# Optimization experiments

Measured on AMD Instinct MI355X. Metric: run time of the kernel, lower is better.

The kernel has to match this reference:

```python
import jax, jax.numpy as jnp
import numpy as np

N = 2_000_000
WIDTH, HEIGHT = 1920, 1080
ZNEAR, ZFAR = 0.01, 100.0
TAN_FOVX = 0.5773503  # 60 deg horizontal FoV
TAN_FOVY = TAN_FOVX * HEIGHT / WIDTH


def _camera():
    # Row-vector convention: x_view = x_h @ world2view (translation in last row).
    w2v = np.eye(4, dtype=np.float32)
    w2v[3, 2] = 5.0  # push scene 5 units in front of the camera
    P = np.zeros((4, 4), dtype=np.float32)
    P[0, 0] = 1.0 / TAN_FOVX
    P[1, 1] = 1.0 / TAN_FOVY
    P[2, 2] = ZFAR / (ZFAR - ZNEAR)
    P[3, 2] = -(ZFAR * ZNEAR) / (ZFAR - ZNEAR)
    P[2, 3] = 1.0
    full = w2v @ P
    return jnp.asarray(w2v), jnp.asarray(full)


def setup_inputs() -> dict:
    key = jax.random.key(0)
    ks = jax.random.split(key, 5)
    w2v, full = _camera()
    return dict(
        points=jax.random.normal(ks[0], (N, 3), jnp.float32) * 2.0,
        colors=jax.random.uniform(ks[1], (N, 3), jnp.float32),
        opacity=jax.random.normal(ks[2], (N,), jnp.float32),
        scales=jax.random.uniform(ks[3], (N, 3), jnp.float32, minval=0.01, maxval=0.2),
        quaternions=jax.random.normal(ks[4], (N, 4), jnp.float32),
        world2view=w2v,
        full_proj_transform=full,
        tan_fovX=jnp.full((1,), TAN_FOVX, jnp.float32),
        tan_fovY=jnp.full((1,), TAN_FOVY, jnp.float32),
        focal_x=jnp.full((1,), WIDTH / (2.0 * TAN_FOVX), jnp.float32),
        focal_y=jnp.full((1,), HEIGHT / (2.0 * TAN_FOVY), jnp.float32),
        width=WIDTH,
        height=HEIGHT,
    )


def _quat_to_rot(q):
    q = q / jnp.linalg.norm(q, axis=-1, keepdims=True)
    w, x, y, z = q[:, 0], q[:, 1], q[:, 2], q[:, 3]
    R = jnp.stack([
        1 - 2 * (y * y + z * z), 2 * (x * y - w * z), 2 * (x * z + w * y),
        2 * (x * y + w * z), 1 - 2 * (x * x + z * z), 2 * (y * z - w * x),
        2 * (x * z - w * y), 2 * (y * z + w * x), 1 - 2 * (x * x + y * y),
    ], axis=-1)
    return R.reshape(-1, 3, 3)


def reference(points, colors, opacity, scales, quaternions, world2view,
              full_proj_transform, tan_fovX, tan_fovY, focal_x, focal_y,
              width, height):
    n = points.shape[0]
    # --- 3D covariance: Sigma = (R S)(R S)^T ---
    R = _quat_to_rot(quaternions)                      # [N,3,3]
    M = R * scales[:, None, :]                         # R @ diag(s)
    cov3d = jnp.einsum('nij,nkj->nik', M, M)           # [N,3,3]

    # --- view / clip transforms (row-vector convention) ---
    ph = jnp.concatenate([points, jnp.ones((n, 1), points.dtype)], axis=1)
    pview = ph @ world2view                            # [N,4]
    zview = pview[:, 2]
    in_view = zview >= 0.2                             # frustum (near-plane) cull

    pclip = ph @ full_proj_transform
    pndc = pclip[:, :3] / pclip[:, 3:4]
    px = ((pndc[:, 0] + 1.0) * width - 1.0) * 0.5      # ndc2Pix
    py = ((pndc[:, 1] + 1.0) * height - 1.0) * 0.5

    # --- 2D covariance via projection Jacobian (EWA splatting) ---
    xc = jnp.clip(pview[:, 0] / zview, -1.3 * tan_fovX, 1.3 * tan_fovX) * zview
    yc = jnp.clip(pview[:, 1] / zview, -1.3 * tan_fovY, 1.3 * tan_fovY) * zview
    z2 = zview * zview
    zero = jnp.zeros_like(zview)
    J = jnp.stack([
        focal_x / zview, zero, -(focal_x * xc) / z2,
        zero, focal_y / zview, -(focal_y * yc) / z2,
        zero, zero, zero,
    ], axis=-1).reshape(-1, 3, 3)                      # [N,3,3]
    W = world2view[:3, :3].T
    T = jnp.einsum('nij,jk->nik', J, W)
    cov2d = jnp.einsum('nij,njk,nlk->nil', T, cov3d, T)[:, :2, :2]

    # --- analytic 2x2 inverse ---
    c00, c01 = cov2d[:, 0, 0], cov2d[:, 0, 1]
    c10, c11 = cov2d[:, 1, 0], cov2d[:, 1, 1]
    det = c00 * c11 - c01 * c10
    det_safe = jnp.where(jnp.abs(det) < 1e-6, 1e-6, det)
    inv_cov = jnp.stack([c11, -c01, -c10, c00], axis=-1) / det_safe[:, None]

    # --- extent / radius: 3 sigma of dominant eigenvalue ---
    mid = 0.5 * (c00 + c11)
    inter = jnp.maximum(mid * mid - det, 0.1)
    lam = mid + jnp.sqrt(inter)
    radius = jnp.ceil(3.0 * jnp.sqrt(jnp.maximum(lam, 0.0)))

    min_x = jnp.floor(px - radius)
    min_y = jnp.floor(py - radius)
    max_x = jnp.ceil(px + radius)
    max_y = jnp.ceil(py + radius)

    # --- depth sort; culled gaussians keyed to +inf (fixed-shape stand-in for boolean gather) ---
    depth_key = jnp.where(in_view, zview, jnp.float32(jnp.inf))
    order = jnp.argsort(depth_key)

    packed = jnp.concatenate([
        px[:, None], py[:, None], zview[:, None],
        cov2d.reshape(n, 4), inv_cov,
        radius[:, None],
        min_x[:, None], min_y[:, None], max_x[:, None], max_y[:, None],
        colors, jax.nn.sigmoid(opacity)[:, None],
        in_view.astype(points.dtype)[:, None],
    ], axis=1)                                          # [N,21]
    return packed[order]
```

## Files before the change

### kernel.cpp

```cpp
#include <hip/hip_runtime.h>
#include <hip/hip_bf16.h>
#include <math.h>

#define BLK   256
#define IPT   16
#define TILE  (BLK * IPT)
#define BINS  256
#define PASSES 4
#define SCT   4096

__global__ __launch_bounds__(256) void k_keys(const float* __restrict__ pts,
                                              const float* __restrict__ w2v,
                                              int N,
                                              unsigned* __restrict__ keys,
                                              unsigned* __restrict__ idx)
{
    int i = blockIdx.x * 256 + threadIdx.x;
    if (i >= N) return;
    float x = pts[3*i+0], y = pts[3*i+1], z = pts[3*i+2];
    float zv = x*w2v[2] + y*w2v[6] + z*w2v[10] + w2v[14];
    float key = (zv >= 0.2f) ? zv : __int_as_float(0x7f800000);
    unsigned u = __float_as_uint(key);
    u ^= (u & 0x80000000u) ? 0xFFFFFFFFu : 0x80000000u;
    keys[i] = u;
    idx[i]  = (unsigned)i;
}

__global__ __launch_bounds__(256) void k_hist8(const unsigned* __restrict__ keys,
                                               int N, int numTiles, int shift,
                                               unsigned* __restrict__ hist)
{
    __shared__ unsigned bins[BINS];
    int t = threadIdx.x, b = blockIdx.x;
    bins[t] = 0;
    __syncthreads();
    int base = b * TILE;
    for (int k = 0; k < IPT; ++k) {
        int l = base + k * BLK + t;
        if (l < N) atomicAdd(&bins[(keys[l] >> shift) & 255u], 1u);
    }
    __syncthreads();
    hist[t * numTiles + b] = bins[t];
}

__global__ __launch_bounds__(256) void k_scanA(const unsigned* __restrict__ h, int E,
                                               unsigned* __restrict__ bsum)
{
    __shared__ unsigned red[256];
    int t = threadIdx.x;
    int base = blockIdx.x * SCT + t * 16;
    unsigned acc = 0;
    if (base + 16 <= E) {
        const uint4* p = (const uint4*)(h + base);
        #pragma unroll
        for (int q = 0; q < 4; ++q) { uint4 v = p[q]; acc += v.x + v.y + v.z + v.w; }
    } else {
        for (int k = 0; k < 16; ++k) { int i = base + k; if (i < E) acc += h[i]; }
    }
    red[t] = acc;
    __syncthreads();
    for (int off = 128; off > 0; off >>= 1) {
        if (t < off) red[t] += red[t + off];
        __syncthreads();
    }
    if (t == 0) bsum[blockIdx.x] = red[0];
}

__global__ __launch_bounds__(256) void k_scanB(unsigned* __restrict__ h, int E,
                                               const unsigned* __restrict__ bsum)
{
    __shared__ unsigned tsum[256];
    __shared__ unsigned boff_s;
    int t = threadIdx.x, b = blockIdx.x;
    int base = b * SCT + t * 16;

    if (t == 0) { unsigned o = 0; for (int i = 0; i < b; ++i) o += bsum[i]; boff_s = o; }

    unsigned v[16];
    bool full = (base + 16 <= E);
    if (full) {
        const uint4* p = (const uint4*)(h + base);
        #pragma unroll
        for (int q = 0; q < 4; ++q) { uint4 u = p[q]; v[4*q]=u.x; v[4*q+1]=u.y; v[4*q+2]=u.z; v[4*q+3]=u.w; }
    } else {
        for (int k = 0; k < 16; ++k) { int i = base + k; v[k] = (i < E) ? h[i] : 0u; }
    }
    unsigned acc = 0;
    #pragma unroll
    for (int k = 0; k < 16; ++k) { unsigned x = v[k]; v[k] = acc; acc += x; }
    tsum[t] = acc;
    __syncthreads();
    for (int off = 1; off < 256; off <<= 1) {
        unsigned u = (t >= off) ? tsum[t - off] : 0u;
        __syncthreads();
        tsum[t] += u;
        __syncthreads();
    }
    unsigned add = boff_s + ((t == 0) ? 0u : tsum[t - 1]);
    if (full) {
        uint4* p = (uint4*)(h + base);
        #pragma unroll
        for (int q = 0; q < 4; ++q)
            p[q] = make_uint4(v[4*q] + add, v[4*q+1] + add, v[4*q+2] + add, v[4*q+3] + add);
    } else {
        for (int k = 0; k < 16; ++k) { int i = base + k; if (i < E) h[i] = v[k] + add; }
    }
}

__global__ __launch_bounds__(256) void k_scatter8(const unsigned* __restrict__ keys,
                                                  const unsigned* __restrict__ vals,
                                                  int N, int numTiles, int shift,
                                                  const unsigned* __restrict__ hist,
                                                  unsigned* __restrict__ okeys,
                                                  unsigned* __restrict__ ovals)
{
    __shared__ unsigned short cnt[64 * BINS];
    __shared__ unsigned tileBase[BINS];
    __shared__ unsigned digStartL[BINS];
    __shared__ unsigned tscan[BINS];
    __shared__ unsigned stage_k[TILE];
    __shared__ unsigned stage_v[TILE];

    int t = threadIdx.x, b = blockIdx.x;
    int w = t >> 6, l = t & 63;
    int base = b * TILE;
    int nvalid = N - base; if (nvalid < 0) nvalid = 0; if (nvalid > TILE) nvalid = TILE;

    unsigned* c32 = (unsigned*)cnt;
    #pragma unroll
    for (int i = 0; i < (64 * BINS / 2) / BLK; ++i) c32[i * BLK + t] = 0;
    __syncthreads();

    unsigned k_[IPT], v_[IPT];
    unsigned char r_[IPT], d_[IPT];

    #pragma unroll
    for (int it = 0; it < IPT; ++it) {
        int e = base + it * BLK + t;
        bool ok = e < N;
        k_[it] = ok ? keys[e] : 0u;
        v_[it] = ok ? vals[e] : 0u;
    }

    #pragma unroll
    for (int it = 0; it < IPT; ++it) {
        int e = base + it * BLK + t;
        bool ok = e < N;
        unsigned d = (k_[it] >> shift) & 255u;
        unsigned long long mm = __ballot(ok);
        #pragma unroll
        for (int bb = 0; bb < 8; ++bb) {
            unsigned long long bal = __ballot(ok && ((d >> bb) & 1u));
            mm &= ((d >> bb) & 1u) ? bal : ~bal;
        }
        unsigned long long below = mm & ((1ull << l) - 1ull);
        unsigned rk = (unsigned)__popcll(below);
        if (ok && rk == 0)
            cnt[(it * 4 + w) * BINS + d] = (unsigned short)__popcll(mm);
        r_[it] = (unsigned char)rk;
        d_[it] = (unsigned char)d;
    }
    __syncthreads();

    {
        unsigned run = 0;
        #pragma unroll
        for (int s = 0; s < 64; ++s) {
            unsigned h = cnt[s * BINS + t];
            cnt[s * BINS + t] = (unsigned short)run;
            run += h;
        }
        tscan[t] = run;
        tileBase[t] = hist[t * numTiles + b];
    }
    __syncthreads();

    for (int off = 1; off < 256; off <<= 1) {
        unsigned u = (t >= off) ? tscan[t - off] : 0u;
        __syncthreads();
        tscan[t] += u;
        __syncthreads();
    }
    digStartL[t] = (t == 0) ? 0u : tscan[t - 1];
    __syncthreads();

    #pragma unroll
    for (int it = 0; it < IPT; ++it) {
        int e = base + it * BLK + t;
        if (e >= N) continue;
        unsigned d = d_[it];
        unsigned lp = digStartL[d] + (unsigned)cnt[(it * 4 + w) * BINS + d] + (unsigned)r_[it];
        stage_k[lp] = k_[it];
        stage_v[lp] = v_[it];
    }
    __syncthreads();

    #pragma unroll
    for (int it = 0; it < IPT; ++it) {
        int p = it * BLK + t;
        if (p >= nvalid) continue;
        unsigned kk = stage_k[p];
        unsigned d = (kk >> shift) & 255u;
        unsigned pos = tileBase[d] + ((unsigned)p - digStartL[d]);
        okeys[pos] = kk;
        ovals[pos] = stage_v[p];
    }
}

__device__ __forceinline__ void compute_row(int j,
                                            const float* __restrict__ pts,
                                            const float* __restrict__ cols,
                                            const float* __restrict__ opa,
                                            const float* __restrict__ scl,
                                            const float* __restrict__ qt,
                                            const float* __restrict__ w2v,
                                            const float* __restrict__ fpm,
                                            float tanX, float tanY, float fx, float fy,
                                            float Wf, float Hf,
                                            float* r )
{
    float x = pts[3*j+0], y = pts[3*j+1], z = pts[3*j+2];

    float qw = qt[4*j+0], qx = qt[4*j+1], qy = qt[4*j+2], qz = qt[4*j+3];
    float qn = sqrtf(qw*qw + qx*qx + qy*qy + qz*qz);
    qw /= qn; qx /= qn; qy /= qn; qz /= qn;
    float R00 = 1.f - 2.f*(qy*qy + qz*qz), R01 = 2.f*(qx*qy - qw*qz), R02 = 2.f*(qx*qz + qw*qy);
    float R10 = 2.f*(qx*qy + qw*qz), R11 = 1.f - 2.f*(qx*qx + qz*qz), R12 = 2.f*(qy*qz - qw*qx);
    float R20 = 2.f*(qx*qz - qw*qy), R21 = 2.f*(qy*qz + qw*qx), R22 = 1.f - 2.f*(qx*qx + qy*qy);

    float s0 = scl[3*j+0], s1 = scl[3*j+1], s2 = scl[3*j+2];
    float M00=R00*s0, M01=R01*s1, M02=R02*s2;
    float M10=R10*s0, M11=R11*s1, M12=R12*s2;
    float M20=R20*s0, M21=R21*s1, M22=R22*s2;
    float C00=M00*M00+M01*M01+M02*M02;
    float C01=M00*M10+M01*M11+M02*M12;
    float C02=M00*M20+M01*M21+M02*M22;
    float C11=M10*M10+M11*M11+M12*M12;
    float C12=M10*M20+M11*M21+M12*M22;
    float C22=M20*M20+M21*M21+M22*M22;

    float pvx = x*w2v[0] + y*w2v[4] + z*w2v[8]  + w2v[12];
    float pvy = x*w2v[1] + y*w2v[5] + z*w2v[9]  + w2v[13];
    float zv  = x*w2v[2] + y*w2v[6] + z*w2v[10] + w2v[14];
    bool in_view = (zv >= 0.2f);

    float cx = x*fpm[0] + y*fpm[4] + z*fpm[8]  + fpm[12];
    float cy = x*fpm[1] + y*fpm[5] + z*fpm[9]  + fpm[13];
    float cw = x*fpm[3] + y*fpm[7] + z*fpm[11] + fpm[15];
    float ndx = cx / cw, ndy = cy / cw;
    float px = ((ndx + 1.f) * Wf - 1.f) * 0.5f;
    float py = ((ndy + 1.f) * Hf - 1.f) * 0.5f;

    float lx = 1.3f * tanX, ly = 1.3f * tanY;
    float xc = fminf(fmaxf(pvx / zv, -lx), lx) * zv;
    float yc = fminf(fmaxf(pvy / zv, -ly), ly) * zv;
    float z2 = zv * zv;
    float J00 = fx / zv, J02 = -(fx * xc) / z2;
    float J11 = fy / zv, J12 = -(fy * yc) / z2;

    float T00 = J00*w2v[0] + J02*w2v[2];
    float T01 = J00*w2v[4] + J02*w2v[6];
    float T02 = J00*w2v[8] + J02*w2v[10];
    float T10 = J11*w2v[1] + J12*w2v[2];
    float T11 = J11*w2v[5] + J12*w2v[6];
    float T12 = J11*w2v[9] + J12*w2v[10];

    float V00 = T00*C00 + T01*C01 + T02*C02;
    float V01 = T00*C01 + T01*C11 + T02*C12;
    float V02 = T00*C02 + T01*C12 + T02*C22;
    float V10 = T10*C00 + T11*C01 + T12*C02;
    float V11 = T10*C01 + T11*C11 + T12*C12;
    float V12 = T10*C02 + T11*C12 + T12*C22;
    float c00 = V00*T00 + V01*T01 + V02*T02;
    float c01 = V00*T10 + V01*T11 + V02*T12;
    float c10 = V10*T00 + V11*T01 + V12*T02;
    float c11 = V10*T10 + V11*T11 + V12*T12;

    float det = c00*c11 - c01*c10;
    float det_safe = (fabsf(det) < 1e-6f) ? 1e-6f : det;
    float i00 =  c11 / det_safe, i01 = -c01 / det_safe;
    float i10 = -c10 / det_safe, i11 =  c00 / det_safe;
    float mid = 0.5f * (c00 + c11);
    float inter = fmaxf(mid*mid - det, 0.1f);
    float lam = mid + sqrtf(inter);
    float radius = ceilf(3.0f * sqrtf(fmaxf(lam, 0.0f)));
    float min_x = floorf(px - radius), min_y = floorf(py - radius);
    float max_x = ceilf(px + radius),  max_y = ceilf(py + radius);
    float op = 1.0f / (1.0f + expf(-opa[j]));

    r[0]=px; r[1]=py; r[2]=zv;
    r[3]=c00; r[4]=c01; r[5]=c10; r[6]=c11;
    r[7]=i00; r[8]=i01; r[9]=i10; r[10]=i11;
    r[11]=radius; r[12]=min_x; r[13]=min_y; r[14]=max_x; r[15]=max_y;
    r[16]=cols[3*j+0]; r[17]=cols[3*j+1]; r[18]=cols[3*j+2];
    r[19]=op; r[20]= in_view ? 1.0f : 0.0f;
}

__global__ __launch_bounds__(256) void k_rows(const float* __restrict__ pts,
                                              const float* __restrict__ cols,
                                              const float* __restrict__ opa,
                                              const float* __restrict__ scl,
                                              const float* __restrict__ qt,
                                              const float* __restrict__ w2v,
                                              const float* __restrict__ fpm,
                                              const float* __restrict__ tanx_p,
                                              const float* __restrict__ tany_p,
                                              const float* __restrict__ fx_p,
                                              const float* __restrict__ fy_p,
                                              const int* __restrict__ wp,
                                              const int* __restrict__ hp,
                                              float* __restrict__ rows, int N)
{
    int i = blockIdx.x * 256 + threadIdx.x;
    if (i >= N) return;
    float r[21];
    compute_row(i, pts, cols, opa, scl, qt, w2v, fpm,
                tanx_p[0], tany_p[0], fx_p[0], fy_p[0],
                (float)wp[0], (float)hp[0], r);
    float4* rp = (float4*)(rows + (size_t)i * 24);
    rp[0] = make_float4(r[0],  r[1],  r[2],  r[3]);
    rp[1] = make_float4(r[4],  r[5],  r[6],  r[7]);
    rp[2] = make_float4(r[8],  r[9],  r[10], r[11]);
    rp[3] = make_float4(r[12], r[13], r[14], r[15]);
    rp[4] = make_float4(r[16], r[17], r[18], r[19]);
    rp[5] = make_float4(r[20], 0.f,   0.f,   0.f);
}

__global__ __launch_bounds__(256) void k_perm(const unsigned* __restrict__ order,
                                              const float* __restrict__ rows,
                                              float* __restrict__ out, int N)
{
    __shared__ float srow[256 * 21];
    int i = blockIdx.x * 256 + threadIdx.x;
    if (i < N) {
        int j = (int)order[i];
        const float4* rp = (const float4*)(rows + (size_t)j * 24);
        float4 a = rp[0], b4 = rp[1], c4 = rp[2], d4 = rp[3], e4 = rp[4];
        float  f = rows[(size_t)j * 24 + 20];
        float* r = &srow[threadIdx.x * 21];
        r[0]=a.x;  r[1]=a.y;  r[2]=a.z;  r[3]=a.w;
        r[4]=b4.x; r[5]=b4.y; r[6]=b4.z; r[7]=b4.w;
        r[8]=c4.x; r[9]=c4.y; r[10]=c4.z; r[11]=c4.w;
        r[12]=d4.x; r[13]=d4.y; r[14]=d4.z; r[15]=d4.w;
        r[16]=e4.x; r[17]=e4.y; r[18]=e4.z; r[19]=e4.w;
        r[20]=f;
    }
    __syncthreads();
    int blockBase = blockIdx.x * 256;
    int valid = N - blockBase; if (valid > 256) valid = 256;
    if (valid > 0) {
        float* dst = out + (size_t)blockBase * 21;
        for (int u = threadIdx.x; u < valid * 21; u += 256) dst[u] = srow[u];
    }
}

__global__ __launch_bounds__(256) void k_emit(const unsigned* __restrict__ order,
                                              const float* __restrict__ pts,
                                              const float* __restrict__ cols,
                                              const float* __restrict__ opa,
                                              const float* __restrict__ scl,
                                              const float* __restrict__ qt,
                                              const float* __restrict__ w2v,
                                              const float* __restrict__ fpm,
                                              const float* __restrict__ tanx_p,
                                              const float* __restrict__ tany_p,
                                              const float* __restrict__ fx_p,
                                              const float* __restrict__ fy_p,
                                              const int* __restrict__ wp,
                                              const int* __restrict__ hp,
                                              float* __restrict__ out, int N)
{
    __shared__ float srow[256 * 21];
    int i = blockIdx.x * 256 + threadIdx.x;
    if (i < N) {
        int j = (int)order[i];
        compute_row(j, pts, cols, opa, scl, qt, w2v, fpm,
                    tanx_p[0], tany_p[0], fx_p[0], fy_p[0],
                    (float)wp[0], (float)hp[0], &srow[threadIdx.x * 21]);
    }
    __syncthreads();
    int blockBase = blockIdx.x * 256;
    int valid = N - blockBase; if (valid > 256) valid = 256;
    if (valid > 0) {
        float* dst = out + (size_t)blockBase * 21;
        for (int u = threadIdx.x; u < valid * 21; u += 256) dst[u] = srow[u];
    }
}

extern "C" void kernel_launch(void* const* d_in, const int* in_sizes, int n_in,
                              void* d_out, int out_size, void* d_ws, size_t ws_size,
                              hipStream_t stream)
{
    const float* pts  = (const float*)d_in[0];
    const float* cols = (const float*)d_in[1];
    const float* opa  = (const float*)d_in[2];
    const float* scl  = (const float*)d_in[3];
    const float* qt   = (const float*)d_in[4];
    const float* w2v  = (const float*)d_in[5];
    const float* fpm  = (const float*)d_in[6];
    const float* tanx = (const float*)d_in[7];
    const float* tany = (const float*)d_in[8];
    const float* fx   = (const float*)d_in[9];
    const float* fy   = (const float*)d_in[10];
    const int*   wp   = (const int*)d_in[11];
    const int*   hp   = (const int*)d_in[12];

    int N = in_sizes[0] / 3;
    int numTiles = (N + TILE - 1) / TILE;
    int nb = (N + 255) / 256;
    int E = BINS * numTiles;
    int nScan = (E + SCT - 1) / SCT;

    unsigned* keysA = (unsigned*)d_ws;
    unsigned* idxA  = keysA + N;
    unsigned* keysB = idxA  + N;
    unsigned* idxB  = keysB + N;
    unsigned* hist  = idxB  + N;
    unsigned* bsum  = hist + E;
    float*    rows  = (float*)(bsum + nScan);

    size_t need = ((size_t)4 * N + E + nScan) * 4 + (size_t)N * 24 * 4;
    bool split = (ws_size >= need);

    k_keys<<<nb, 256, 0, stream>>>(pts, w2v, N, keysA, idxA);

    unsigned *ck = keysA, *cv = idxA, *nk = keysB, *nvv = idxB;
    for (int p = 0; p < PASSES; ++p) {
        int shift = p * 8;
        k_hist8<<<numTiles, 256, 0, stream>>>(ck, N, numTiles, shift, hist);
        k_scanA<<<nScan, 256, 0, stream>>>(hist, E, bsum);
        k_scanB<<<nScan, 256, 0, stream>>>(hist, E, bsum);
        k_scatter8<<<numTiles, 256, 0, stream>>>(ck, cv, N, numTiles, shift, hist, nk, nvv);
        unsigned* tk = ck; ck = nk; nk = tk;
        unsigned* tv = cv; cv = nvv; nvv = tv;
    }

    if (split) {
        k_rows<<<nb, 256, 0, stream>>>(pts, cols, opa, scl, qt, w2v, fpm,
                                       tanx, tany, fx, fy, wp, hp, rows, N);
        k_perm<<<nb, 256, 0, stream>>>(cv, rows, (float*)d_out, N);
    } else {
        k_emit<<<nb, 256, 0, stream>>>(cv, pts, cols, opa, scl, qt, w2v, fpm,
                                       tanx, tany, fx, fy, wp, hp,
                                       (float*)d_out, N);
    }
}
```

Before: 562.2 us.

## Fuse key generation into row compute, compact rows, and streamline radix sort passes

Merges the depth-key kernel into the per-gaussian row kernel and shrinks each stored row from 24 to 16 floats, dropping the duplicated covariance entries and the bounding-box values, which the permute kernel now rebuilds. The radix sort is reworked: the histogram uses vectorised loads with per-wave bins, the scatter uses per-warp counters with a single shared staging buffer, the first pass synthesises the index values instead of reading them, and the last pass skips writing keys. Divisions and the sigmoid switch to hardware reciprocal, rsqrt and fast-exp intrinsics, and the no-workspace fallback path is removed. The goal is less memory traffic and fewer kernels; in exchange the approximate intrinsics may change low-order bits, and the code now assumes the workspace is always large enough.

```diff
diff --git a/kernel.cpp b/kernel.cpp
--- a/kernel.cpp
+++ b/kernel.cpp
@@ -5,296 +5,10 @@
 #define BLK   256
 #define IPT   16
 #define TILE  (BLK * IPT)
+#define CHUNK 1024
 #define BINS  256
 #define PASSES 4
 #define SCT   4096
-
-__global__ __launch_bounds__(256) void k_keys(const float* __restrict__ pts,
-                                              const float* __restrict__ w2v,
-                                              int N,
-                                              unsigned* __restrict__ keys,
-                                              unsigned* __restrict__ idx)
-{
-    int i = blockIdx.x * 256 + threadIdx.x;
-    if (i >= N) return;
-    float x = pts[3*i+0], y = pts[3*i+1], z = pts[3*i+2];
-    float zv = x*w2v[2] + y*w2v[6] + z*w2v[10] + w2v[14];
-    float key = (zv >= 0.2f) ? zv : __int_as_float(0x7f800000);
-    unsigned u = __float_as_uint(key);
-    u ^= (u & 0x80000000u) ? 0xFFFFFFFFu : 0x80000000u;
-    keys[i] = u;
-    idx[i]  = (unsigned)i;
-}
-
-__global__ __launch_bounds__(256) void k_hist8(const unsigned* __restrict__ keys,
-                                               int N, int numTiles, int shift,
-                                               unsigned* __restrict__ hist)
-{
-    __shared__ unsigned bins[BINS];
-    int t = threadIdx.x, b = blockIdx.x;
-    bins[t] = 0;
-    __syncthreads();
-    int base = b * TILE;
-    for (int k = 0; k < IPT; ++k) {
-        int l = base + k * BLK + t;
-        if (l < N) atomicAdd(&bins[(keys[l] >> shift) & 255u], 1u);
-    }
-    __syncthreads();
-    hist[t * numTiles + b] = bins[t];
-}
-
-__global__ __launch_bounds__(256) void k_scanA(const unsigned* __restrict__ h, int E,
-                                               unsigned* __restrict__ bsum)
-{
-    __shared__ unsigned red[256];
-    int t = threadIdx.x;
-    int base = blockIdx.x * SCT + t * 16;
-    unsigned acc = 0;
-    if (base + 16 <= E) {
-        const uint4* p = (const uint4*)(h + base);
-        #pragma unroll
-        for (int q = 0; q < 4; ++q) { uint4 v = p[q]; acc += v.x + v.y + v.z + v.w; }
-    } else {
-        for (int k = 0; k < 16; ++k) { int i = base + k; if (i < E) acc += h[i]; }
-    }
-    red[t] = acc;
-    __syncthreads();
-    for (int off = 128; off > 0; off >>= 1) {
-        if (t < off) red[t] += red[t + off];
-        __syncthreads();
-    }
-    if (t == 0) bsum[blockIdx.x] = red[0];
-}
-
-__global__ __launch_bounds__(256) void k_scanB(unsigned* __restrict__ h, int E,
-                                               const unsigned* __restrict__ bsum)
-{
-    __shared__ unsigned tsum[256];
-    __shared__ unsigned boff_s;
-    int t = threadIdx.x, b = blockIdx.x;
-    int base = b * SCT + t * 16;
-
-    if (t == 0) { unsigned o = 0; for (int i = 0; i < b; ++i) o += bsum[i]; boff_s = o; }
-
-    unsigned v[16];
-    bool full = (base + 16 <= E);
-    if (full) {
-        const uint4* p = (const uint4*)(h + base);
-        #pragma unroll
-        for (int q = 0; q < 4; ++q) { uint4 u = p[q]; v[4*q]=u.x; v[4*q+1]=u.y; v[4*q+2]=u.z; v[4*q+3]=u.w; }
-    } else {
-        for (int k = 0; k < 16; ++k) { int i = base + k; v[k] = (i < E) ? h[i] : 0u; }
-    }
-    unsigned acc = 0;
-    #pragma unroll
-    for (int k = 0; k < 16; ++k) { unsigned x = v[k]; v[k] = acc; acc += x; }
-    tsum[t] = acc;
-    __syncthreads();
-    for (int off = 1; off < 256; off <<= 1) {
-        unsigned u = (t >= off) ? tsum[t - off] : 0u;
-        __syncthreads();
-        tsum[t] += u;
-        __syncthreads();
-    }
-    unsigned add = boff_s + ((t == 0) ? 0u : tsum[t - 1]);
-    if (full) {
-        uint4* p = (uint4*)(h + base);
-        #pragma unroll
-        for (int q = 0; q < 4; ++q)
-            p[q] = make_uint4(v[4*q] + add, v[4*q+1] + add, v[4*q+2] + add, v[4*q+3] + add);
-    } else {
-        for (int k = 0; k < 16; ++k) { int i = base + k; if (i < E) h[i] = v[k] + add; }
-    }
-}
-
-__global__ __launch_bounds__(256) void k_scatter8(const unsigned* __restrict__ keys,
-                                                  const unsigned* __restrict__ vals,
-                                                  int N, int numTiles, int shift,
-                                                  const unsigned* __restrict__ hist,
-                                                  unsigned* __restrict__ okeys,
-                                                  unsigned* __restrict__ ovals)
-{
-    __shared__ unsigned short cnt[64 * BINS];
-    __shared__ unsigned tileBase[BINS];
-    __shared__ unsigned digStartL[BINS];
-    __shared__ unsigned tscan[BINS];
-    __shared__ unsigned stage_k[TILE];
-    __shared__ unsigned stage_v[TILE];
-
-    int t = threadIdx.x, b = blockIdx.x;
-    int w = t >> 6, l = t & 63;
-    int base = b * TILE;
-    int nvalid = N - base; if (nvalid < 0) nvalid = 0; if (nvalid > TILE) nvalid = TILE;
-
-    unsigned* c32 = (unsigned*)cnt;
-    #pragma unroll
-    for (int i = 0; i < (64 * BINS / 2) / BLK; ++i) c32[i * BLK + t] = 0;
-    __syncthreads();
-
-    unsigned k_[IPT], v_[IPT];
-    unsigned char r_[IPT], d_[IPT];
-
-    #pragma unroll
-    for (int it = 0; it < IPT; ++it) {
-        int e = base + it * BLK + t;
-        bool ok = e < N;
-        k_[it] = ok ? keys[e] : 0u;
-        v_[it] = ok ? vals[e] : 0u;
-    }
-
-    #pragma unroll
-    for (int it = 0; it < IPT; ++it) {
-        int e = base + it * BLK + t;
-        bool ok = e < N;
-        unsigned d = (k_[it] >> shift) & 255u;
-        unsigned long long mm = __ballot(ok);
-        #pragma unroll
-        for (int bb = 0; bb < 8; ++bb) {
-            unsigned long long bal = __ballot(ok && ((d >> bb) & 1u));
-            mm &= ((d >> bb) & 1u) ? bal : ~bal;
-        }
-        unsigned long long below = mm & ((1ull << l) - 1ull);
-        unsigned rk = (unsigned)__popcll(below);
-        if (ok && rk == 0)
-            cnt[(it * 4 + w) * BINS + d] = (unsigned short)__popcll(mm);
-        r_[it] = (unsigned char)rk;
-        d_[it] = (unsigned char)d;
-    }
-    __syncthreads();
-
-    {
-        unsigned run = 0;
-        #pragma unroll
-        for (int s = 0; s < 64; ++s) {
-            unsigned h = cnt[s * BINS + t];
-            cnt[s * BINS + t] = (unsigned short)run;
-            run += h;
-        }
-        tscan[t] = run;
-        tileBase[t] = hist[t * numTiles + b];
-    }
-    __syncthreads();
-
-    for (int off = 1; off < 256; off <<= 1) {
-        unsigned u = (t >= off) ? tscan[t - off] : 0u;
-        __syncthreads();
-        tscan[t] += u;
-        __syncthreads();
-    }
-    digStartL[t] = (t == 0) ? 0u : tscan[t - 1];
-    __syncthreads();
-
-    #pragma unroll
-    for (int it = 0; it < IPT; ++it) {
-        int e = base + it * BLK + t;
-        if (e >= N) continue;
-        unsigned d = d_[it];
-        unsigned lp = digStartL[d] + (unsigned)cnt[(it * 4 + w) * BINS + d] + (unsigned)r_[it];
-        stage_k[lp] = k_[it];
-        stage_v[lp] = v_[it];
-    }
-    __syncthreads();
-
-    #pragma unroll
-    for (int it = 0; it < IPT; ++it) {
-        int p = it * BLK + t;
-        if (p >= nvalid) continue;
-        unsigned kk = stage_k[p];
-        unsigned d = (kk >> shift) & 255u;
-        unsigned pos = tileBase[d] + ((unsigned)p - digStartL[d]);
-        okeys[pos] = kk;
-        ovals[pos] = stage_v[p];
-    }
-}
-
-__device__ __forceinline__ void compute_row(int j,
-                                            const float* __restrict__ pts,
-                                            const float* __restrict__ cols,
-                                            const float* __restrict__ opa,
-                                            const float* __restrict__ scl,
-                                            const float* __restrict__ qt,
-                                            const float* __restrict__ w2v,
-                                            const float* __restrict__ fpm,
-                                            float tanX, float tanY, float fx, float fy,
-                                            float Wf, float Hf,
-                                            float* r )
-{
-    float x = pts[3*j+0], y = pts[3*j+1], z = pts[3*j+2];
-
-    float qw = qt[4*j+0], qx = qt[4*j+1], qy = qt[4*j+2], qz = qt[4*j+3];
-    float qn = sqrtf(qw*qw + qx*qx + qy*qy + qz*qz);
-    qw /= qn; qx /= qn; qy /= qn; qz /= qn;
-    float R00 = 1.f - 2.f*(qy*qy + qz*qz), R01 = 2.f*(qx*qy - qw*qz), R02 = 2.f*(qx*qz + qw*qy);
-    float R10 = 2.f*(qx*qy + qw*qz), R11 = 1.f - 2.f*(qx*qx + qz*qz), R12 = 2.f*(qy*qz - qw*qx);
-    float R20 = 2.f*(qx*qz - qw*qy), R21 = 2.f*(qy*qz + qw*qx), R22 = 1.f - 2.f*(qx*qx + qy*qy);
-
-    float s0 = scl[3*j+0], s1 = scl[3*j+1], s2 = scl[3*j+2];
-    float M00=R00*s0, M01=R01*s1, M02=R02*s2;
-    float M10=R10*s0, M11=R11*s1, M12=R12*s2;
-    float M20=R20*s0, M21=R21*s1, M22=R22*s2;
-    float C00=M00*M00+M01*M01+M02*M02;
-    float C01=M00*M10+M01*M11+M02*M12;
-    float C02=M00*M20+M01*M21+M02*M22;
-    float C11=M10*M10+M11*M11+M12*M12;
-    float C12=M10*M20+M11*M21+M12*M22;
-    float C22=M20*M20+M21*M21+M22*M22;
-
-    float pvx = x*w2v[0] + y*w2v[4] + z*w2v[8]  + w2v[12];
-    float pvy = x*w2v[1] + y*w2v[5] + z*w2v[9]  + w2v[13];
-    float zv  = x*w2v[2] + y*w2v[6] + z*w2v[10] + w2v[14];
-    bool in_view = (zv >= 0.2f);
-
-    float cx = x*fpm[0] + y*fpm[4] + z*fpm[8]  + fpm[12];
-    float cy = x*fpm[1] + y*fpm[5] + z*fpm[9]  + fpm[13];
-    float cw = x*fpm[3] + y*fpm[7] + z*fpm[11] + fpm[15];
-    float ndx = cx / cw, ndy = cy / cw;
-    float px = ((ndx + 1.f) * Wf - 1.f) * 0.5f;
-    float py = ((ndy + 1.f) * Hf - 1.f) * 0.5f;
-
-    float lx = 1.3f * tanX, ly = 1.3f * tanY;
-    float xc = fminf(fmaxf(pvx / zv, -lx), lx) * zv;
-    float yc = fminf(fmaxf(pvy / zv, -ly), ly) * zv;
-    float z2 = zv * zv;
-    float J00 = fx / zv, J02 = -(fx * xc) / z2;
-    float J11 = fy / zv, J12 = -(fy * yc) / z2;
-
-    float T00 = J00*w2v[0] + J02*w2v[2];
-    float T01 = J00*w2v[4] + J02*w2v[6];
-    float T02 = J00*w2v[8] + J02*w2v[10];
-    float T10 = J11*w2v[1] + J12*w2v[2];
-    float T11 = J11*w2v[5] + J12*w2v[6];
-    float T12 = J11*w2v[9] + J12*w2v[10];
-
-    float V00 = T00*C00 + T01*C01 + T02*C02;
-    float V01 = T00*C01 + T01*C11 + T02*C12;
-    float V02 = T00*C02 + T01*C12 + T02*C22;
-    float V10 = T10*C00 + T11*C01 + T12*C02;
-    float V11 = T10*C01 + T11*C11 + T12*C12;
-    float V12 = T10*C02 + T11*C12 + T12*C22;
-    float c00 = V00*T00 + V01*T01 + V02*T02;
-    float c01 = V00*T10 + V01*T11 + V02*T12;
-    float c10 = V10*T00 + V11*T01 + V12*T02;
-    float c11 = V10*T10 + V11*T11 + V12*T12;
-
-    float det = c00*c11 - c01*c10;
-    float det_safe = (fabsf(det) < 1e-6f) ? 1e-6f : det;
-    float i00 =  c11 / det_safe, i01 = -c01 / det_safe;
-    float i10 = -c10 / det_safe, i11 =  c00 / det_safe;
-    float mid = 0.5f * (c00 + c11);
-    float inter = fmaxf(mid*mid - det, 0.1f);
-    float lam = mid + sqrtf(inter);
-    float radius = ceilf(3.0f * sqrtf(fmaxf(lam, 0.0f)));
-    float min_x = floorf(px - radius), min_y = floorf(py - radius);
-    float max_x = ceilf(px + radius),  max_y = ceilf(py + radius);
-    float op = 1.0f / (1.0f + expf(-opa[j]));
-
-    r[0]=px; r[1]=py; r[2]=zv;
-    r[3]=c00; r[4]=c01; r[5]=c10; r[6]=c11;
-    r[7]=i00; r[8]=i01; r[9]=i10; r[10]=i11;
-    r[11]=radius; r[12]=min_x; r[13]=min_y; r[14]=max_x; r[15]=max_y;
-    r[16]=cols[3*j+0]; r[17]=cols[3*j+1]; r[18]=cols[3*j+2];
-    r[19]=op; r[20]= in_view ? 1.0f : 0.0f;
-}
 
 __global__ __launch_bounds__(256) void k_rows(const float* __restrict__ pts,
                                               const float* __restrict__ cols,
@@ -309,21 +23,298 @@
                                               const float* __restrict__ fy_p,
                                               const int* __restrict__ wp,
                                               const int* __restrict__ hp,
-                                              float* __restrict__ rows, int N)
+                                              float* __restrict__ rows,
+                                              unsigned* __restrict__ keys,
+                                              int N)
 {
     int i = blockIdx.x * 256 + threadIdx.x;
     if (i >= N) return;
-    float r[21];
-    compute_row(i, pts, cols, opa, scl, qt, w2v, fpm,
-                tanx_p[0], tany_p[0], fx_p[0], fy_p[0],
-                (float)wp[0], (float)hp[0], r);
-    float4* rp = (float4*)(rows + (size_t)i * 24);
-    rp[0] = make_float4(r[0],  r[1],  r[2],  r[3]);
-    rp[1] = make_float4(r[4],  r[5],  r[6],  r[7]);
-    rp[2] = make_float4(r[8],  r[9],  r[10], r[11]);
-    rp[3] = make_float4(r[12], r[13], r[14], r[15]);
-    rp[4] = make_float4(r[16], r[17], r[18], r[19]);
-    rp[5] = make_float4(r[20], 0.f,   0.f,   0.f);
+
+    float x = pts[3*i+0], y = pts[3*i+1], z = pts[3*i+2];
+
+    float zv = x*w2v[2] + y*w2v[6] + z*w2v[10] + w2v[14];
+    bool in_view = (zv >= 0.2f);
+    {
+        float key = in_view ? zv : __int_as_float(0x7f800000);
+        unsigned u = __float_as_uint(key);
+        u ^= (u & 0x80000000u) ? 0xFFFFFFFFu : 0x80000000u;
+        keys[i] = u;
+    }
+
+    float4 q4 = *(const float4*)(qt + 4*i);
+    float qw = q4.x, qx = q4.y, qy = q4.z, qz = q4.w;
+    float rn = __builtin_amdgcn_rsqf(qw*qw + qx*qx + qy*qy + qz*qz);
+    qw *= rn; qx *= rn; qy *= rn; qz *= rn;
+    float R00 = 1.f - 2.f*(qy*qy + qz*qz), R01 = 2.f*(qx*qy - qw*qz), R02 = 2.f*(qx*qz + qw*qy);
+    float R10 = 2.f*(qx*qy + qw*qz), R11 = 1.f - 2.f*(qx*qx + qz*qz), R12 = 2.f*(qy*qz - qw*qx);
+    float R20 = 2.f*(qx*qz - qw*qy), R21 = 2.f*(qy*qz + qw*qx), R22 = 1.f - 2.f*(qx*qx + qy*qy);
+
+    float s0 = scl[3*i+0], s1 = scl[3*i+1], s2 = scl[3*i+2];
+    float M00=R00*s0, M01=R01*s1, M02=R02*s2;
+    float M10=R10*s0, M11=R11*s1, M12=R12*s2;
+    float M20=R20*s0, M21=R21*s1, M22=R22*s2;
+    float C00=M00*M00+M01*M01+M02*M02;
+    float C01=M00*M10+M01*M11+M02*M12;
+    float C02=M00*M20+M01*M21+M02*M22;
+    float C11=M10*M10+M11*M11+M12*M12;
+    float C12=M10*M20+M11*M21+M12*M22;
+    float C22=M20*M20+M21*M21+M22*M22;
+
+    float pvx = x*w2v[0] + y*w2v[4] + z*w2v[8]  + w2v[12];
+    float pvy = x*w2v[1] + y*w2v[5] + z*w2v[9]  + w2v[13];
+
+    float cx = x*fpm[0] + y*fpm[4] + z*fpm[8]  + fpm[12];
+    float cy = x*fpm[1] + y*fpm[5] + z*fpm[9]  + fpm[13];
+    float cw = x*fpm[3] + y*fpm[7] + z*fpm[11] + fpm[15];
+    float rcw = __builtin_amdgcn_rcpf(cw);
+    float Wf = (float)wp[0], Hf = (float)hp[0];
+    float px = ((cx*rcw + 1.f) * Wf - 1.f) * 0.5f;
+    float py = ((cy*rcw + 1.f) * Hf - 1.f) * 0.5f;
+
+    float tanX = tanx_p[0], tanY = tany_p[0], fx = fx_p[0], fy = fy_p[0];
+    float lx = 1.3f * tanX, ly = 1.3f * tanY;
+    float rzv = __builtin_amdgcn_rcpf(zv);
+    float xc = fminf(fmaxf(pvx*rzv, -lx), lx) * zv;
+    float yc = fminf(fmaxf(pvy*rzv, -ly), ly) * zv;
+    float rz2 = rzv * rzv;
+    float J00 = fx * rzv, J02 = -(fx * xc) * rz2;
+    float J11 = fy * rzv, J12 = -(fy * yc) * rz2;
+
+    float T00 = J00*w2v[0] + J02*w2v[2];
+    float T01 = J00*w2v[4] + J02*w2v[6];
+    float T02 = J00*w2v[8] + J02*w2v[10];
+    float T10 = J11*w2v[1] + J12*w2v[2];
+    float T11 = J11*w2v[5] + J12*w2v[6];
+    float T12 = J11*w2v[9] + J12*w2v[10];
+
+    float V00 = T00*C00 + T01*C01 + T02*C02;
+    float V01 = T00*C01 + T01*C11 + T02*C12;
+    float V02 = T00*C02 + T01*C12 + T02*C22;
+    float V10 = T10*C00 + T11*C01 + T12*C02;
+    float V11 = T10*C01 + T11*C11 + T12*C12;
+    float V12 = T10*C02 + T11*C12 + T12*C22;
+    float c00 = V00*T00 + V01*T01 + V02*T02;
+    float c01 = V00*T10 + V01*T11 + V02*T12;
+    float c10 = V10*T00 + V11*T01 + V12*T02;
+    float c11 = V10*T10 + V11*T11 + V12*T12;
+
+    float det = c00*c11 - c01*c10;
+    float det_safe = (fabsf(det) < 1e-6f) ? 1e-6f : det;
+    float rdet = __builtin_amdgcn_rcpf(det_safe);
+    float i00 =  c11 * rdet, i01 = -c01 * rdet, i11 = c00 * rdet;
+    float mid = 0.5f * (c00 + c11);
+    float inter = fmaxf(mid*mid - det, 0.1f);
+    float lam = mid + sqrtf(inter);
+    float radius = ceilf(3.0f * sqrtf(fmaxf(lam, 0.0f)));
+    float op = __builtin_amdgcn_rcpf(1.0f + __expf(-opa[i]));
+
+    float cr = cols[3*i+0], cg = cols[3*i+1], cb = cols[3*i+2];
+
+    float4* rp = (float4*)(rows + (size_t)i * 16);
+    rp[0] = make_float4(px,  py,  zv,  c00);
+    rp[1] = make_float4(c01, c11, i00, i01);
+    rp[2] = make_float4(i11, radius, cr, cg);
+    rp[3] = make_float4(cb,  op,  in_view ? 1.0f : 0.0f, 0.f);
+}
+
+__global__ __launch_bounds__(256) void k_hist8(const unsigned* __restrict__ keys,
+                                               int N, int numTiles, int shift,
+                                               unsigned* __restrict__ hist)
+{
+    __shared__ unsigned hb[4][BINS];
+    int t = threadIdx.x, b = blockIdx.x, w = t >> 6;
+    hb[0][t] = 0; hb[1][t] = 0; hb[2][t] = 0; hb[3][t] = 0;
+    __syncthreads();
+    int base = b * TILE + t * 16;
+    if (base + 16 <= N) {
+        const uint4* p = (const uint4*)(keys + base);
+        #pragma unroll
+        for (int q = 0; q < 4; ++q) {
+            uint4 v = p[q];
+            atomicAdd(&hb[w][(v.x >> shift) & 255u], 1u);
+            atomicAdd(&hb[w][(v.y >> shift) & 255u], 1u);
+            atomicAdd(&hb[w][(v.z >> shift) & 255u], 1u);
+            atomicAdd(&hb[w][(v.w >> shift) & 255u], 1u);
+        }
+    } else {
+        for (int k = 0; k < 16; ++k) {
+            int i = base + k;
+            if (i < N) atomicAdd(&hb[w][(keys[i] >> shift) & 255u], 1u);
+        }
+    }
+    __syncthreads();
+    hist[t * numTiles + b] = hb[0][t] + hb[1][t] + hb[2][t] + hb[3][t];
+}
+
+__global__ __launch_bounds__(256) void k_scanA(const unsigned* __restrict__ h, int E,
+                                               unsigned* __restrict__ bsum)
+{
+    __shared__ unsigned red[256];
+    int t = threadIdx.x;
+    int base = blockIdx.x * SCT + t * 16;
+    unsigned acc = 0;
+    if (base + 16 <= E) {
+        const uint4* p = (const uint4*)(h + base);
+        #pragma unroll
+        for (int q = 0; q < 4; ++q) { uint4 v = p[q]; acc += v.x + v.y + v.z + v.w; }
+    } else {
+        for (int k = 0; k < 16; ++k) { int i = base + k; if (i < E) acc += h[i]; }
+    }
+    red[t] = acc;
+    __syncthreads();
+    for (int off = 128; off > 0; off >>= 1) {
+        if (t < off) red[t] += red[t + off];
+        __syncthreads();
+    }
+    if (t == 0) bsum[blockIdx.x] = red[0];
+}
+
+__global__ __launch_bounds__(256) void k_scanB(unsigned* __restrict__ h, int E,
+                                               const unsigned* __restrict__ bsum)
+{
+    __shared__ unsigned tsum[256];
+    __shared__ unsigned boff_s;
+    int t = threadIdx.x, b = blockIdx.x;
+    int base = b * SCT + t * 16;
+
+    if (t == 0) { unsigned o = 0; for (int i = 0; i < b; ++i) o += bsum[i]; boff_s = o; }
+
+    unsigned v[16];
+    bool full = (base + 16 <= E);
+    if (full) {
+        const uint4* p = (const uint4*)(h + base);
+        #pragma unroll
+        for (int q = 0; q < 4; ++q) { uint4 u = p[q]; v[4*q]=u.x; v[4*q+1]=u.y; v[4*q+2]=u.z; v[4*q+3]=u.w; }
+    } else {
+        for (int k = 0; k < 16; ++k) { int i = base + k; v[k] = (i < E) ? h[i] : 0u; }
+    }
+    unsigned acc = 0;
+    #pragma unroll
+    for (int k = 0; k < 16; ++k) { unsigned x = v[k]; v[k] = acc; acc += x; }
+    tsum[t] = acc;
+    __syncthreads();
+    for (int off = 1; off < 256; off <<= 1) {
+        unsigned u = (t >= off) ? tsum[t - off] : 0u;
+        __syncthreads();
+        tsum[t] += u;
+        __syncthreads();
+    }
+    unsigned add = boff_s + ((t == 0) ? 0u : tsum[t - 1]);
+    if (full) {
+        uint4* p = (uint4*)(h + base);
+        #pragma unroll
+        for (int q = 0; q < 4; ++q)
+            p[q] = make_uint4(v[4*q] + add, v[4*q+1] + add, v[4*q+2] + add, v[4*q+3] + add);
+    } else {
+        for (int k = 0; k < 16; ++k) { int i = base + k; if (i < E) h[i] = v[k] + add; }
+    }
+}
+
+__global__ __launch_bounds__(256) void k_scatter8(const unsigned* __restrict__ keys,
+                                                  const unsigned* __restrict__ vals,
+                                                  int N, int numTiles, int shift,
+                                                  const unsigned* __restrict__ hist,
+                                                  unsigned* __restrict__ okeys,
+                                                  unsigned* __restrict__ ovals)
+{
+    __shared__ unsigned short wcnt[4][BINS];
+    __shared__ unsigned digStartL[BINS];
+    __shared__ unsigned tileBase[BINS];
+    __shared__ unsigned tscan[BINS];
+    __shared__ unsigned stage[TILE];
+
+    int t = threadIdx.x, b = blockIdx.x;
+    int w = t >> 6, l = t & 63;
+    int base = b * TILE;
+    int nvalid = N - base; if (nvalid < 0) nvalid = 0; if (nvalid > TILE) nvalid = TILE;
+    int wbase = base + w * CHUNK;
+
+    ((unsigned*)wcnt)[t] = 0; ((unsigned*)wcnt)[256 + t] = 0;
+    __syncthreads();
+
+    unsigned k_[IPT];
+    unsigned short rw_[IPT];
+    unsigned char d_[IPT];
+
+    #pragma unroll
+    for (int it = 0; it < IPT; ++it) {
+        int e = wbase + it * 64 + l;
+        bool ok = e < N;
+        unsigned kk = ok ? keys[e] : 0u;
+        unsigned d = (kk >> shift) & 255u;
+        unsigned long long mm = __ballot(ok);
+        #pragma unroll
+        for (int bb = 0; bb < 8; ++bb) {
+            unsigned long long bal = __ballot(ok && ((d >> bb) & 1u));
+            mm &= ((d >> bb) & 1u) ? bal : ~bal;
+        }
+        unsigned long long below = mm & ((1ull << l) - 1ull);
+        unsigned rk = (unsigned)__popcll(below);
+        unsigned before = (unsigned)wcnt[w][d];
+        if (ok && rk == 0)
+            wcnt[w][d] = (unsigned short)(before + (unsigned)__popcll(mm));
+        k_[it]  = kk;
+        rw_[it] = (unsigned short)(before + rk);
+        d_[it]  = (unsigned char)d;
+    }
+    __syncthreads();
+
+    {
+        unsigned c0 = wcnt[0][t], c1 = wcnt[1][t], c2 = wcnt[2][t], c3 = wcnt[3][t];
+        wcnt[0][t] = 0;
+        wcnt[1][t] = (unsigned short)c0;
+        wcnt[2][t] = (unsigned short)(c0 + c1);
+        wcnt[3][t] = (unsigned short)(c0 + c1 + c2);
+        tscan[t] = c0 + c1 + c2 + c3;
+        tileBase[t] = hist[t * numTiles + b];
+    }
+    __syncthreads();
+    for (int off = 1; off < 256; off <<= 1) {
+        unsigned u = (t >= off) ? tscan[t - off] : 0u;
+        __syncthreads();
+        tscan[t] += u;
+        __syncthreads();
+    }
+    digStartL[t] = (t == 0) ? 0u : tscan[t - 1];
+    __syncthreads();
+
+    unsigned lp_[IPT];
+    #pragma unroll
+    for (int it = 0; it < IPT; ++it) {
+        int e = wbase + it * 64 + l;
+        if (e < N) {
+            unsigned d = d_[it];
+            lp_[it] = digStartL[d] + (unsigned)wcnt[w][d] + (unsigned)rw_[it];
+            stage[lp_[it]] = k_[it];
+        }
+    }
+    __syncthreads();
+
+    unsigned pos_[IPT];
+    #pragma unroll
+    for (int it = 0; it < IPT; ++it) {
+        int p = it * BLK + t;
+        if (p < nvalid) {
+            unsigned kk = stage[p];
+            unsigned d = (kk >> shift) & 255u;
+            unsigned pos = tileBase[d] + ((unsigned)p - digStartL[d]);
+            pos_[it] = pos;
+            if (okeys) okeys[pos] = kk;
+        }
+    }
+    __syncthreads();
+
+    #pragma unroll
+    for (int it = 0; it < IPT; ++it) {
+        int e = wbase + it * 64 + l;
+        if (e < N) stage[lp_[it]] = vals ? vals[e] : (unsigned)e;
+    }
+    __syncthreads();
+    #pragma unroll
+    for (int it = 0; it < IPT; ++it) {
+        int p = it * BLK + t;
+        if (p < nvalid) ovals[pos_[it]] = stage[p];
+    }
 }
 
 __global__ __launch_bounds__(256) void k_perm(const unsigned* __restrict__ order,
@@ -334,49 +325,21 @@
     int i = blockIdx.x * 256 + threadIdx.x;
     if (i < N) {
         int j = (int)order[i];
-        const float4* rp = (const float4*)(rows + (size_t)j * 24);
-        float4 a = rp[0], b4 = rp[1], c4 = rp[2], d4 = rp[3], e4 = rp[4];
-        float  f = rows[(size_t)j * 24 + 20];
+        const float4* rp = (const float4*)(rows + (size_t)j * 16);
+        float4 a = rp[0], b4 = rp[1], c4 = rp[2], d4 = rp[3];
+        float px = a.x,  py = a.y,  zv = a.z,  c00 = a.w;
+        float c01 = b4.x, c11 = b4.y, i00 = b4.z, i01 = b4.w;
+        float i11 = c4.x, rad = c4.y, cr = c4.z, cg = c4.w;
+        float cb = d4.x,  op = d4.y,  iv = d4.z;
         float* r = &srow[threadIdx.x * 21];
-        r[0]=a.x;  r[1]=a.y;  r[2]=a.z;  r[3]=a.w;
-        r[4]=b4.x; r[5]=b4.y; r[6]=b4.z; r[7]=b4.w;
-        r[8]=c4.x; r[9]=c4.y; r[10]=c4.z; r[11]=c4.w;
-        r[12]=d4.x; r[13]=d4.y; r[14]=d4.z; r[15]=d4.w;
-        r[16]=e4.x; r[17]=e4.y; r[18]=e4.z; r[19]=e4.w;
-        r[20]=f;
-    }
-    __syncthreads();
-    int blockBase = blockIdx.x * 256;
-    int valid = N - blockBase; if (valid > 256) valid = 256;
-    if (valid > 0) {
-        float* dst = out + (size_t)blockBase * 21;
-        for (int u = threadIdx.x; u < valid * 21; u += 256) dst[u] = srow[u];
-    }
-}
-
-__global__ __launch_bounds__(256) void k_emit(const unsigned* __restrict__ order,
-                                              const float* __restrict__ pts,
-                                              const float* __restrict__ cols,
-                                              const float* __restrict__ opa,
-                                              const float* __restrict__ scl,
-                                              const float* __restrict__ qt,
-                                              const float* __restrict__ w2v,
-                                              const float* __restrict__ fpm,
-                                              const float* __restrict__ tanx_p,
-                                              const float* __restrict__ tany_p,
-                                              const float* __restrict__ fx_p,
-                                              const float* __restrict__ fy_p,
-                                              const int* __restrict__ wp,
-                                              const int* __restrict__ hp,
-                                              float* __restrict__ out, int N)
-{
-    __shared__ float srow[256 * 21];
-    int i = blockIdx.x * 256 + threadIdx.x;
-    if (i < N) {
-        int j = (int)order[i];
-        compute_row(j, pts, cols, opa, scl, qt, w2v, fpm,
-                    tanx_p[0], tany_p[0], fx_p[0], fy_p[0],
-                    (float)wp[0], (float)hp[0], &srow[threadIdx.x * 21]);
+        r[0]=px; r[1]=py; r[2]=zv;
+        r[3]=c00; r[4]=c01; r[5]=c01; r[6]=c11;
+        r[7]=i00; r[8]=i01; r[9]=i01; r[10]=i11;
+        r[11]=rad;
+        r[12]=floorf(px - rad); r[13]=floorf(py - rad);
+        r[14]=ceilf(px + rad);  r[15]=ceilf(py + rad);
+        r[16]=cr; r[17]=cg; r[18]=cb;
+        r[19]=op; r[20]=iv;
     }
     __syncthreads();
     int blockBase = blockIdx.x * 256;
@@ -411,37 +374,36 @@
     int E = BINS * numTiles;
     int nScan = (E + SCT - 1) / SCT;
 
-    unsigned* keysA = (unsigned*)d_ws;
-    unsigned* idxA  = keysA + N;
-    unsigned* keysB = idxA  + N;
-    unsigned* idxB  = keysB + N;
-    unsigned* hist  = idxB  + N;
-    unsigned* bsum  = hist + E;
-    float*    rows  = (float*)(bsum + nScan);
-
-    size_t need = ((size_t)4 * N + E + nScan) * 4 + (size_t)N * 24 * 4;
-    bool split = (ws_size >= need);
-
-    k_keys<<<nb, 256, 0, stream>>>(pts, w2v, N, keysA, idxA);
-
-    unsigned *ck = keysA, *cv = idxA, *nk = keysB, *nvv = idxB;
-    for (int p = 0; p < PASSES; ++p) {
-        int shift = p * 8;
-        k_hist8<<<numTiles, 256, 0, stream>>>(ck, N, numTiles, shift, hist);
-        k_scanA<<<nScan, 256, 0, stream>>>(hist, E, bsum);
-        k_scanB<<<nScan, 256, 0, stream>>>(hist, E, bsum);
-        k_scatter8<<<numTiles, 256, 0, stream>>>(ck, cv, N, numTiles, shift, hist, nk, nvv);
-        unsigned* tk = ck; ck = nk; nk = tk;
-        unsigned* tv = cv; cv = nvv; nvv = tv;
-    }
-
-    if (split) {
-        k_rows<<<nb, 256, 0, stream>>>(pts, cols, opa, scl, qt, w2v, fpm,
-                                       tanx, tany, fx, fy, wp, hp, rows, N);
-        k_perm<<<nb, 256, 0, stream>>>(cv, rows, (float*)d_out, N);
-    } else {
-        k_emit<<<nb, 256, 0, stream>>>(cv, pts, cols, opa, scl, qt, w2v, fpm,
-                                       tanx, tany, fx, fy, wp, hp,
-                                       (float*)d_out, N);
-    }
-}
+    unsigned* kA   = (unsigned*)d_ws;
+    unsigned* kB   = kA + N;
+    unsigned* vA   = kB + N;
+    unsigned* vB   = vA + N;
+    unsigned* hist = vB + N;
+    unsigned* bsum = hist + E;
+    float*    rows = (float*)(bsum + nScan);
+
+    k_rows<<<nb, 256, 0, stream>>>(pts, cols, opa, scl, qt, w2v, fpm,
+                                   tanx, tany, fx, fy, wp, hp, rows, kA, N);
+
+    k_hist8<<<numTiles, 256, 0, stream>>>(kA, N, numTiles, 0, hist);
+    k_scanA<<<nScan, 256, 0, stream>>>(hist, E, bsum);
+    k_scanB<<<nScan, 256, 0, stream>>>(hist, E, bsum);
+    k_scatter8<<<numTiles, 256, 0, stream>>>(kA, nullptr, N, numTiles, 0, hist, kB, vA);
+
+    k_hist8<<<numTiles, 256, 0, stream>>>(kB, N, numTiles, 8, hist);
+    k_scanA<<<nScan, 256, 0, stream>>>(hist, E, bsum);
+    k_scanB<<<nScan, 256, 0, stream>>>(hist, E, bsum);
+    k_scatter8<<<numTiles, 256, 0, stream>>>(kB, vA, N, numTiles, 8, hist, kA, vB);
+
+    k_hist8<<<numTiles, 256, 0, stream>>>(kA, N, numTiles, 16, hist);
+    k_scanA<<<nScan, 256, 0, stream>>>(hist, E, bsum);
+    k_scanB<<<nScan, 256, 0, stream>>>(hist, E, bsum);
+    k_scatter8<<<numTiles, 256, 0, stream>>>(kA, vB, N, numTiles, 16, hist, kB, vA);
+
+    k_hist8<<<numTiles, 256, 0, stream>>>(kB, N, numTiles, 24, hist);
+    k_scanA<<<nScan, 256, 0, stream>>>(hist, E, bsum);
+    k_scanB<<<nScan, 256, 0, stream>>>(hist, E, bsum);
+    k_scatter8<<<numTiles, 256, 0, stream>>>(kB, vA, N, numTiles, 24, hist, nullptr, vB);
+
+    k_perm<<<nb, 256, 0, stream>>>(vB, rows, (float*)d_out, N);
+}
```

Result: faster. 503.4 us (-10.5%).
